# Kernel optimization log

Measured on AMD Instinct MI355X. Metric: run time of the kernel, lower is better.

## Reference

```python
import jax, jax.numpy as jnp
import numpy as np

B, C, W, H, HEADS = 8, 512, 32, 32, 8
DH = C // HEADS  # 64
N = W * H        # 1024


def setup_inputs() -> dict:
    key = jax.random.key(0)
    ks = jax.random.split(key, 10)
    s = 1.0 / np.sqrt(C)
    return {
        "x": jax.random.normal(ks[0], (B, C, W, H), jnp.float32),
        "d": jax.random.normal(ks[1], (B, C, W, H), jnp.float32),
        "Wq": jax.random.normal(ks[2], (C, C), jnp.float32) * s,
        "bq": jnp.zeros((C,), jnp.float32),
        "Wk": jax.random.normal(ks[3], (C, C), jnp.float32) * s,
        "bk": jnp.zeros((C,), jnp.float32),
        "Wv": jax.random.normal(ks[4], (C, C), jnp.float32) * s,
        "bv": jnp.zeros((C,), jnp.float32),
        "rel_h": jax.random.normal(ks[5], (1, HEADS, DH, 1, H), jnp.float32),
        "rel_w": jax.random.normal(ks[6], (1, HEADS, DH, W, 1), jnp.float32),
    }


def reference(x, d, Wq, bq, Wk, bk, Wv, bv, rel_h, rel_w):
    b, c, w, h = x.shape
    heads = rel_h.shape[1]
    dh = c // heads
    n = w * h

    def proj(t, Wt, bt):
        # 1x1 conv == per-pixel channel matmul; reshape to [B, heads, dh, N]
        y = jnp.einsum('bchw,oc->bohw', t, Wt) + bt[None, :, None, None]
        return y.reshape(b, heads, dh, n)

    q = proj(x, Wq, bq)
    k = proj(d, Wk, bk)
    v = proj(d, Wv, bv)

    # content-content: q^T k -> [B, h, N, N]
    cc = jnp.einsum('bhdn,bhdm->bhnm', q, k)
    # content-position: (rel_h + rel_w) broadcast -> [1, h, dh, N], then pos^T @ q
    pos = (rel_h + rel_w).reshape(heads, dh, n)
    cp = jnp.einsum('hdm,bhdn->bhmn', pos, q)

    attn = jax.nn.softmax(cc + cp, axis=-1)  # [B, h, N, N]
    # out = v @ attn^T : out[b,h,d,i] = sum_j v[b,h,d,j] * attn[b,h,i,j]
    out = jnp.einsum('bhdj,bhij->bhdi', v, attn)
    return out.reshape(b, c, w, h)
```

## Files before the change

kernel.cpp:

```cpp
#include <hip/hip_runtime.h>

typedef unsigned short u16;
typedef _Float16 f16x8 __attribute__((ext_vector_type(8)));
typedef __fp16 hf16x2 __attribute__((ext_vector_type(2)));
typedef float f32x4 __attribute__((ext_vector_type(4)));
typedef float f32x16 __attribute__((ext_vector_type(16)));

#define NB 8
#define NC 512
#define NHD 8
#define DH 64
#define NN 1024
#define LOG2E 1.4426950408889634f

__device__ __forceinline__ u16 f2h(float f) {
    union { _Float16 h; u16 u; } v; v.h = (_Float16)f;
    return v.u;
}

__global__ __launch_bounds__(256) void k_prep(
    const float* __restrict__ x, const float* __restrict__ d,
    const float* __restrict__ Wq, const float* __restrict__ Wk, const float* __restrict__ Wv,
    const float* __restrict__ relh, const float* __restrict__ relw,
    u16* __restrict__ xt, u16* __restrict__ dt,
    u16* __restrict__ wq, u16* __restrict__ wk, u16* __restrict__ wv,
    u16* __restrict__ ps) {
    __shared__ float tile[64][65];
    int id = blockIdx.x, t = threadIdx.x;
    if (id < 2048) {
        int nb = (id & 15) * 64;
        int cb = ((id >> 4) & 7) * 64;
        int z = id >> 7;
        int b = z & 7;
        const float* src = (z >> 3) ? d : x;
        u16* ot = (z >> 3) ? dt : xt;
        {
            int crow = t >> 2, n0 = (t & 3) * 16;
            const float* g = src + ((size_t)(b * NC + cb + crow)) * NN + nb + n0;
#pragma unroll
            for (int k = 0; k < 16; k += 4) {
                float4 v = *(const float4*)(g + k);
                tile[crow][n0 + k + 0] = v.x;
                tile[crow][n0 + k + 1] = v.y;
                tile[crow][n0 + k + 2] = v.z;
                tile[crow][n0 + k + 3] = v.w;
            }
        }
        __syncthreads();
        {
            int nrow = t >> 2, c0 = (t & 3) * 16;
            union { u16 s[16]; uint4 v[2]; } uh;
#pragma unroll
            for (int k = 0; k < 16; ++k) uh.s[k] = f2h(tile[c0 + k][nrow]);
            size_t oidx = ((size_t)(b * NN + nb + nrow)) * NC + cb + c0;
            *(uint4*)(ot + oidx)     = uh.v[0];
            *(uint4*)(ot + oidx + 8) = uh.v[1];
        }
    } else if (id < 5120) {
        int j = id - 2048;
        int m = j >> 10;
        int i = (j & 1023) * 256 + t;
        const float* src = (m == 0) ? Wq : (m == 1) ? Wk : Wv;
        u16* dst = (m == 0) ? wq : (m == 1) ? wk : wv;
        dst[i] = f2h(src[i]);
    } else {
        int idx = (id - 5120) * 256 + t;
        int dd = idx & 63;
        int i  = (idx >> 6) & 1023;
        int h  = idx >> 16;
        float f = relh[(h * 64 + dd) * 32 + (i & 31)] + relw[(h * 64 + dd) * 32 + (i >> 5)];
        ps[(h * 1024 + i) * 64 + dd] = f2h(f);
    }
}

__global__ __launch_bounds__(256) void k_proj(
    const u16* __restrict__ xt, const u16* __restrict__ dt,
    const u16* __restrict__ wq, const u16* __restrict__ wk, const u16* __restrict__ wv,
    const float* __restrict__ bq, const float* __restrict__ bk, const float* __restrict__ bv,
    u16* __restrict__ qt_o, u16* __restrict__ kt_o, u16* __restrict__ v_o) {
    __shared__ u16 Asm[128 * 32];
    __shared__ u16 Bsm[128 * 32];

    int p = blockIdx.z % 3;
    int b = blockIdx.z / 3;
    const u16 *Ap, *Bp;
    const float* bias;
    u16* Oq;
    if (p == 0)      { Ap = wq; Bp = xt; bias = bq; Oq = qt_o; }
    else if (p == 1) { Ap = wk; Bp = dt; bias = bk; Oq = kt_o; }
    else             { Ap = wv; Bp = dt; bias = bv; Oq = v_o; }
    Bp += (size_t)b * NN * NC;
    float oscale = (p == 0) ? LOG2E : 1.0f;

    int obase = blockIdx.x * 128;
    int nbase = blockIdx.y * 128;
    int t = threadIdx.x, wave = t >> 6, quad = (t & 63) >> 4, l15 = t & 15;
    int wr = (wave >> 1) * 64, wc = (wave & 1) * 64;

    f32x4 acc[4][4];
#pragma unroll
    for (int fo = 0; fo < 4; ++fo)
#pragma unroll
        for (int fn = 0; fn < 4; ++fn)
#pragma unroll
            for (int r = 0; r < 4; ++r) acc[fo][fn][r] = 0.f;

    for (int kk = 0; kk < NC; kk += 32) {
        __syncthreads();
#pragma unroll
        for (int u = 0; u < 2; ++u) {
            int c = u * 256 + t;
            int row = c >> 2, part = c & 3;
            __builtin_amdgcn_global_load_lds(
                (const __attribute__((address_space(1))) void*)(Ap + (size_t)(obase + row) * NC + kk + part * 8),
                (__attribute__((address_space(3))) void*)(Asm + (size_t)(u * 256 + wave * 64) * 8), 16, 0, 0);
            __builtin_amdgcn_global_load_lds(
                (const __attribute__((address_space(1))) void*)(Bp + (size_t)(nbase + row) * NC + kk + part * 8),
                (__attribute__((address_space(3))) void*)(Bsm + (size_t)(u * 256 + wave * 64) * 8), 16, 0, 0);
        }
        __syncthreads();

        f16x8 af[4], bfr[4];
#pragma unroll
        for (int fo = 0; fo < 4; ++fo) af[fo] = *(const f16x8*)&Asm[(wr + fo * 16 + l15) * 32 + quad * 8];
#pragma unroll
        for (int fn = 0; fn < 4; ++fn) bfr[fn] = *(const f16x8*)&Bsm[(wc + fn * 16 + l15) * 32 + quad * 8];
#pragma unroll
        for (int fo = 0; fo < 4; ++fo)
#pragma unroll
            for (int fn = 0; fn < 4; ++fn)
                acc[fo][fn] = __builtin_amdgcn_mfma_f32_16x16x32_f16(af[fo], bfr[fn], acc[fo][fn], 0, 0, 0);
    }

#pragma unroll
    for (int fo = 0; fo < 4; ++fo) {
#pragma unroll
        for (int fn = 0; fn < 4; ++fn) {
            int o0 = obase + wr + fo * 16 + quad * 4;
            int n = nbase + wc + fn * 16 + l15;
            if (p < 2) {
                union { u16 s[4]; uint2 v2; } uh;
#pragma unroll
                for (int r = 0; r < 4; ++r) uh.s[r] = f2h((acc[fo][fn][r] + bias[o0 + r]) * oscale);
                int head = o0 >> 6, dd0 = o0 & 63;
                size_t idx = (((size_t)(b * NHD + head) * NN) + n) * DH + dd0;
                *(uint2*)&Oq[idx] = uh.v2;
            } else {
#pragma unroll
                for (int r = 0; r < 4; ++r) {
                    int o = o0 + r;
                    int head = o >> 6, dd = o & 63;
                    Oq[((size_t)(b * NHD + head) * DH + dd) * NN + n] = f2h(acc[fo][fn][r] + bias[o]);
                }
            }
        }
    }
}

__global__ __launch_bounds__(256, 2) void k_attn(
    const u16* __restrict__ qt, const u16* __restrict__ kt,
    const u16* __restrict__ v_, const u16* __restrict__ pos,
    float* __restrict__ out) {
    __shared__ u16 Bs[128 * 132];
    __shared__ u16 Vt[64 * 132];
    __shared__ u16 Pt[4 * 32 * 68];

    int n = blockIdx.x;
    int g = n & 63;
    int ib = n >> 6;
    int head = g & 7, b = g >> 3;

    int t = threadIdx.x, ws = t >> 6, lane = t & 63, h = lane >> 5, l31 = lane & 31;
    size_t bh = (size_t)(b * NHD + head);
    const u16* qb = qt + bh * NN * DH;
    const u16* kb = kt + bh * NN * DH;
    const u16* vb = v_ + bh * DH * NN;
    const u16* pb = pos + (size_t)head * NN * DH;
    int i0 = ib * 128;
    int iglob = i0 + ws * 32 + l31;

    f16x8 qf[8];
#pragma unroll
    for (int ks = 0; ks < 4; ++ks) qf[ks] = *(const f16x8*)&qb[(size_t)iglob * DH + ks * 16 + h * 8];
#pragma unroll
    for (int ks = 4; ks < 8; ++ks) qf[ks] = *(const f16x8*)&pb[(size_t)iglob * DH + (ks - 4) * 16 + h * 8];

    f32x16 oacc[2];
#pragma unroll
    for (int df = 0; df < 2; ++df)
#pragma unroll
        for (int r = 0; r < 16; ++r) oacc[df][r] = 0.f;
    float m_ = -__builtin_inff(), l_ = 0.f;
    int ptb = ws * 32 * 68;

    for (int jc = 0; jc < NN; jc += 128) {
        __syncthreads();
#pragma unroll
        for (int u = 0; u < 8; ++u) {
            int c = u * 256 + t;
            int row = c >> 4, gg = c & 15;
            const u16* src = (gg < 8) ? &kb[(size_t)(jc + row) * DH + gg * 8]
                                      : &qb[(size_t)(jc + row) * DH + (gg - 8) * 8];
            *(uint4*)&Bs[row * 132 + gg * 8] = *(const uint4*)src;
        }
#pragma unroll
        for (int u = 0; u < 4; ++u) {
            int c = u * 256 + t;
            int row = c >> 4, gg = c & 15;
            *(uint4*)&Vt[row * 132 + gg * 8] = *(const uint4*)&vb[(size_t)row * NN + jc + gg * 8];
        }
        __syncthreads();

        f32x16 sacc[4];
#pragma unroll
        for (int jf = 0; jf < 4; ++jf)
#pragma unroll
            for (int r = 0; r < 16; ++r) sacc[jf][r] = 0.f;
#pragma unroll
        for (int jf = 0; jf < 4; ++jf)
#pragma unroll
            for (int ks = 0; ks < 8; ++ks) {
                f16x8 af = *(const f16x8*)&Bs[(jf * 32 + l31) * 132 + ks * 16 + h * 8];
                sacc[jf] = __builtin_amdgcn_mfma_f32_32x32x16_f16(af, qf[ks], sacc[jf], 0, 0, 0);
            }

        float mloc = -__builtin_inff();
#pragma unroll
        for (int jf = 0; jf < 4; ++jf)
#pragma unroll
            for (int r = 0; r < 16; ++r) mloc = fmaxf(mloc, sacc[jf][r]);
        mloc = fmaxf(mloc, __shfl_xor(mloc, 32));
        if (__any(mloc > m_)) {
            float mnew = fmaxf(m_, mloc);
            float alpha = __builtin_amdgcn_exp2f(m_ - mnew);
            m_ = mnew;
#pragma unroll
            for (int df = 0; df < 2; ++df)
#pragma unroll
                for (int r = 0; r < 16; ++r) oacc[df][r] *= alpha;
            l_ *= alpha;
        }
        float lsum = 0.f;
#pragma unroll
        for (int jf = 0; jf < 4; ++jf)
#pragma unroll
            for (int r = 0; r < 16; ++r) {
                float pv = __builtin_amdgcn_exp2f(sacc[jf][r] - m_);
                sacc[jf][r] = pv;
                lsum += pv;
            }
        lsum += __shfl_xor(lsum, 32);
        l_ += lsum;

#pragma unroll
        for (int half = 0; half < 2; ++half) {
#pragma unroll
            for (int jf = 0; jf < 2; ++jf) {
                int jfg = half * 2 + jf;
#pragma unroll
                for (int mm = 0; mm < 4; ++mm) {
                    union { hf16x2 v; unsigned u; } p0, p1;
                    p0.v = __builtin_amdgcn_cvt_pkrtz(sacc[jfg][mm * 4 + 0], sacc[jfg][mm * 4 + 1]);
                    p1.v = __builtin_amdgcn_cvt_pkrtz(sacc[jfg][mm * 4 + 2], sacc[jfg][mm * 4 + 3]);
                    uint2 w; w.x = p0.u; w.y = p1.u;
                    *(uint2*)&Pt[ptb + l31 * 68 + jf * 32 + 4 * h + 8 * mm] = w;
                }
            }
#pragma unroll
            for (int jw = 0; jw < 4; ++jw) {
                f16x8 pf = *(const f16x8*)&Pt[ptb + l31 * 68 + jw * 16 + h * 8];
#pragma unroll
                for (int df = 0; df < 2; ++df) {
                    f16x8 vf = *(const f16x8*)&Vt[(df * 32 + l31) * 132 + half * 64 + jw * 16 + h * 8];
                    oacc[df] = __builtin_amdgcn_mfma_f32_32x32x16_f16(vf, pf, oacc[df], 0, 0, 0);
                }
            }
        }
    }

    float li = 1.0f / l_;
#pragma unroll
    for (int df = 0; df < 2; ++df)
#pragma unroll
        for (int r = 0; r < 16; ++r) {
            int dd = df * 32 + (r & 3) + 8 * (r >> 2) + 4 * h;
            out[((size_t)(b * NC) + head * DH + dd) * NN + i0 + ws * 32 + l31] = oacc[df][r] * li;
        }
}

#define SXT  (8u * 1024u * 512u * 2u)
#define SW   (512u * 512u * 2u)
#define SQT  SXT
#define SPOS (8u * 1024u * 64u * 2u)

#define OFF_XT   (0u)
#define OFF_DT   (OFF_XT + SXT)
#define OFF_WQ   (OFF_DT + SXT)
#define OFF_WK   (OFF_WQ + SW)
#define OFF_WV   (OFF_WK + SW)
#define OFF_QT   (OFF_WV + SW)
#define OFF_KT   (OFF_QT + SQT)
#define OFF_V    (OFF_KT + SQT)
#define OFF_POS  (OFF_V + SQT)

extern "C" void kernel_launch(void* const* d_in, const int* in_sizes, int n_in,
                              void* d_out, int out_size, void* d_ws, size_t ws_size,
                              hipStream_t stream) {
    const float* x   = (const float*)d_in[0];
    const float* d   = (const float*)d_in[1];
    const float* Wq  = (const float*)d_in[2];
    const float* bq  = (const float*)d_in[3];
    const float* Wk  = (const float*)d_in[4];
    const float* bk  = (const float*)d_in[5];
    const float* Wv  = (const float*)d_in[6];
    const float* bv  = (const float*)d_in[7];
    const float* rh  = (const float*)d_in[8];
    const float* rw  = (const float*)d_in[9];

    char* ws = (char*)d_ws;
    u16* xt = (u16*)(ws + OFF_XT);
    u16* dt = (u16*)(ws + OFF_DT);
    u16* wq = (u16*)(ws + OFF_WQ);
    u16* wk = (u16*)(ws + OFF_WK);
    u16* wv = (u16*)(ws + OFF_WV);
    u16* qt = (u16*)(ws + OFF_QT);
    u16* kt = (u16*)(ws + OFF_KT);
    u16* v_ = (u16*)(ws + OFF_V);
    u16* ps = (u16*)(ws + OFF_POS);

    k_prep<<<7168, 256, 0, stream>>>(x, d, Wq, Wk, Wv, rh, rw, xt, dt, wq, wk, wv, ps);
    k_proj<<<dim3(4, 8, 24), 256, 0, stream>>>(xt, dt, wq, wk, wv, bq, bk, bv, qt, kt, v_);
    k_attn<<<512, 256, 0, stream>>>(qt, kt, v_, ps, (float*)d_out);
}
```

Baseline: 167.8 us.

## Repack softmax probabilities in registers via permlane32_swap instead of LDS

Removes the per-wave LDS staging buffer used to transpose the softmax probabilities into the MFMA B-operand layout. It builds the operand in registers with cvt_pkrtz plus permlane32_swap, cutting LDS writes and reads and the LDS footprint. It also raises wave priority around the MFMA sections. It applies a lazy rescale, so the running max only updates when the new max exceeds it by more than 8 in log2 units. That risks fp16 overflow of unnormalised probabilities and accumulators if values grow up to 2^8 before rescaling.

```diff
diff --git a/kernel.cpp b/kernel.cpp
--- a/kernel.cpp
+++ b/kernel.cpp
@@ -5,6 +5,7 @@
 typedef __fp16 hf16x2 __attribute__((ext_vector_type(2)));
 typedef float f32x4 __attribute__((ext_vector_type(4)));
 typedef float f32x16 __attribute__((ext_vector_type(16)));
+typedef unsigned uint2v __attribute__((ext_vector_type(2)));
 
 #define NB 8
 #define NC 512
@@ -163,7 +164,6 @@
     float* __restrict__ out) {
     __shared__ u16 Bs[128 * 132];
     __shared__ u16 Vt[64 * 132];
-    __shared__ u16 Pt[4 * 32 * 68];
 
     int n = blockIdx.x;
     int g = n & 63;
@@ -191,7 +191,6 @@
 #pragma unroll
         for (int r = 0; r < 16; ++r) oacc[df][r] = 0.f;
     float m_ = -__builtin_inff(), l_ = 0.f;
-    int ptb = ws * 32 * 68;
 
     for (int jc = 0; jc < NN; jc += 128) {
         __syncthreads();
@@ -216,6 +215,7 @@
         for (int jf = 0; jf < 4; ++jf)
 #pragma unroll
             for (int r = 0; r < 16; ++r) sacc[jf][r] = 0.f;
+        __builtin_amdgcn_s_setprio(1);
 #pragma unroll
         for (int jf = 0; jf < 4; ++jf)
 #pragma unroll
@@ -223,6 +223,7 @@
                 f16x8 af = *(const f16x8*)&Bs[(jf * 32 + l31) * 132 + ks * 16 + h * 8];
                 sacc[jf] = __builtin_amdgcn_mfma_f32_32x32x16_f16(af, qf[ks], sacc[jf], 0, 0, 0);
             }
+        __builtin_amdgcn_s_setprio(0);
 
         float mloc = -__builtin_inff();
 #pragma unroll
@@ -230,7 +231,7 @@
 #pragma unroll
             for (int r = 0; r < 16; ++r) mloc = fmaxf(mloc, sacc[jf][r]);
         mloc = fmaxf(mloc, __shfl_xor(mloc, 32));
-        if (__any(mloc > m_)) {
+        if (__any(mloc - m_ > 8.f)) {
             float mnew = fmaxf(m_, mloc);
             float alpha = __builtin_amdgcn_exp2f(m_ - mnew);
             m_ = mnew;
@@ -252,30 +253,29 @@
         lsum += __shfl_xor(lsum, 32);
         l_ += lsum;
 
-#pragma unroll
-        for (int half = 0; half < 2; ++half) {
-#pragma unroll
-            for (int jf = 0; jf < 2; ++jf) {
-                int jfg = half * 2 + jf;
-#pragma unroll
-                for (int mm = 0; mm < 4; ++mm) {
-                    union { hf16x2 v; unsigned u; } p0, p1;
-                    p0.v = __builtin_amdgcn_cvt_pkrtz(sacc[jfg][mm * 4 + 0], sacc[jfg][mm * 4 + 1]);
-                    p1.v = __builtin_amdgcn_cvt_pkrtz(sacc[jfg][mm * 4 + 2], sacc[jfg][mm * 4 + 3]);
-                    uint2 w; w.x = p0.u; w.y = p1.u;
-                    *(uint2*)&Pt[ptb + l31 * 68 + jf * 32 + 4 * h + 8 * mm] = w;
-                }
-            }
-#pragma unroll
-            for (int jw = 0; jw < 4; ++jw) {
-                f16x8 pf = *(const f16x8*)&Pt[ptb + l31 * 68 + jw * 16 + h * 8];
-#pragma unroll
-                for (int df = 0; df < 2; ++df) {
-                    f16x8 vf = *(const f16x8*)&Vt[(df * 32 + l31) * 132 + half * 64 + jw * 16 + h * 8];
-                    oacc[df] = __builtin_amdgcn_mfma_f32_32x32x16_f16(vf, pf, oacc[df], 0, 0, 0);
-                }
-            }
-        }
+        __builtin_amdgcn_s_setprio(1);
+#pragma unroll
+        for (int jw = 0; jw < 8; ++jw) {
+            int jf = jw >> 1, r0 = (jw & 1) * 8;
+            union { hf16x2 v; unsigned u; } a0, a1, b0, b1;
+            a0.v = __builtin_amdgcn_cvt_pkrtz(sacc[jf][r0 + 0], sacc[jf][r0 + 1]);
+            a1.v = __builtin_amdgcn_cvt_pkrtz(sacc[jf][r0 + 2], sacc[jf][r0 + 3]);
+            b0.v = __builtin_amdgcn_cvt_pkrtz(sacc[jf][r0 + 4], sacc[jf][r0 + 5]);
+            b1.v = __builtin_amdgcn_cvt_pkrtz(sacc[jf][r0 + 6], sacc[jf][r0 + 7]);
+            uint2v s0 = __builtin_amdgcn_permlane32_swap(a0.u, b0.u, false, false);
+            uint2v s1 = __builtin_amdgcn_permlane32_swap(a1.u, b1.u, false, false);
+            union { unsigned w[4]; f16x8 f; } pf;
+            pf.w[0] = s0.x;
+            pf.w[1] = s1.x;
+            pf.w[2] = s0.y;
+            pf.w[3] = s1.y;
+#pragma unroll
+            for (int df = 0; df < 2; ++df) {
+                f16x8 vf = *(const f16x8*)&Vt[(df * 32 + l31) * 132 + jw * 16 + h * 8];
+                oacc[df] = __builtin_amdgcn_mfma_f32_32x32x16_f16(vf, pf.f, oacc[df], 0, 0, 0);
+            }
+        }
+        __builtin_amdgcn_s_setprio(0);
     }
 
     float li = 1.0f / l_;
```

New measurement: 165.2 us. Within noise of the previous version (-1.5%).
